# Optimization experiments

Hardware: AMD Instinct MI355X
Metric: run time of the kernel (lower is better)

Reference implementation:

```python
import jax, jax.numpy as jnp
import numpy as np
from jax import lax

B, N, C, T = 32, 1000, 32, 24
K, F_CHEB, F_TIME = 3, 64, 64


def setup_inputs() -> dict:
    key = jax.random.key(0)
    ks = jax.random.split(key, 7)
    return {
        "x": jax.random.normal(ks[0], (B, N, C, T), dtype=jnp.float32),
        "cheb_T": jax.random.normal(ks[1], (K, N, N), dtype=jnp.float32) * (1.0 / np.sqrt(N)),
        "Theta": jax.random.normal(ks[2], (K, C, F_CHEB), dtype=jnp.float32) * 0.1,
        "time_w": jax.random.normal(ks[3], (F_TIME, F_CHEB, 1, 3), dtype=jnp.float32) * 0.05,
        "time_b": jax.random.normal(ks[4], (F_TIME,), dtype=jnp.float32) * 0.05,
        "res_w": jax.random.normal(ks[5], (F_TIME, C, 1, 1), dtype=jnp.float32) * 0.1,
        "res_b": jax.random.normal(ks[6], (F_TIME,), dtype=jnp.float32) * 0.05,
    }


def _conv2d(x, w, stride_t, pad_t):
    # x: [B, Cin, N, T] (NCHW with H=nodes, W=time), w: [Cout, Cin, kh, kw]
    return lax.conv_general_dilated(
        x, w, window_strides=(1, stride_t), padding=((0, 0), (pad_t, pad_t)),
        dimension_numbers=("NCHW", "OIHW", "NCHW"))


def reference(x, cheb_T, Theta, time_w, time_b, res_w, res_b):
    # ChebConv: rhs_k[b,n,c,t] = sum_m T_k[m,n] x[b,m,c,t]; out = sum_k rhs_k @ Theta_k
    # Fused over all timesteps and polynomial orders in one einsum.
    spatial = jax.nn.relu(
        jnp.einsum("knm,bmct,kcf->bnft", cheb_T, x, Theta))  # [B,N,F_cheb,T]
    # time conv over the T axis (kernel (1,3), pad (0,1), stride (1,1))
    h = spatial.transpose(0, 2, 1, 3)  # [B,F_cheb,N,T]
    tc = _conv2d(h, time_w, 1, 1) + time_b[None, :, None, None]
    tc = jnp.tanh(tc) * jax.nn.sigmoid(tc)  # wave-net gating
    # 1x1 residual conv on the raw input (Dropout output in source is unused)
    res = _conv2d(x.transpose(0, 2, 1, 3), res_w, 1, 0) + res_b[None, :, None, None]
    out = (res + tc).transpose(0, 2, 1, 3)  # [B,N,F_time,T]
    return out
```

## Files before the change

kernel.cpp:

```cpp
#include <hip/hip_runtime.h>
#include <math.h>

typedef __attribute__((ext_vector_type(4))) float f32x4;
typedef __attribute__((ext_vector_type(16))) float f32x16;
typedef __attribute__((ext_vector_type(8))) short s16x8;
typedef __attribute__((ext_vector_type(8))) unsigned short u16x8;
typedef __attribute__((ext_vector_type(4))) unsigned short u16x4;

#define NB 32
#define NN 1000
#define NT 24
#define NP 1024
#define TCN 768

#define GLOAD16(g, l) __builtin_amdgcn_global_load_lds( \
    (const __attribute__((address_space(1))) unsigned int*)(g), \
    (__attribute__((address_space(3))) unsigned int*)(l), 16, 0, 0)

__device__ __forceinline__ unsigned short f2bf(float f){
  union { float fv; unsigned int u; } v; v.fv = f;
  unsigned int r = v.u + 0x7FFFu + ((v.u >> 16) & 1u);
  return (unsigned short)(r >> 16);
}

__global__ void k0_cheb(const float* __restrict__ cheb, unsigned short* __restrict__ cbT){
  int idx = blockIdx.x * 256 + threadIdx.x;
  int base = idx << 2;
  int m = base & (NP - 1);
  int r = base >> 10;
  int n = r & (NP - 1);
  int k = r >> 10;
  u16x4 o = (u16x4){0,0,0,0};
  if (n < NN && m < NN){
    if (m + 3 < NN){
      f32x4 v = *(const f32x4*)(cheb + ((size_t)k*NN + n)*NN + m);
      o[0] = f2bf(v[0]); o[1] = f2bf(v[1]); o[2] = f2bf(v[2]); o[3] = f2bf(v[3]);
    } else {
      #pragma unroll
      for (int i = 0; i < 4; ++i)
        if (m + i < NN) o[i] = f2bf(cheb[((size_t)k*NN + n)*NN + m + i]);
    }
  }
  *(u16x4*)(cbT + base) = o;
}

__global__ __launch_bounds__(256) void k0_x(const float* __restrict__ x,
                     unsigned short* __restrict__ xbT, unsigned short* __restrict__ xt2){
  __shared__ unsigned short tile[64*770];
  const int b  = blockIdx.x >> 4;
  const int m0 = (blockIdx.x & 15) << 6;
  const int tid = threadIdx.x;
  for (int i = tid; i < 64*192; i += 256){
    int mi = i / 192, c4 = (i - mi*192) << 2;
    f32x4 v = (f32x4){0.f,0.f,0.f,0.f};
    if (m0 + mi < NN) v = *(const f32x4*)(x + (size_t)(b*NN + m0 + mi)*768 + c4);
    unsigned short* tp = tile + mi*770 + c4;
    tp[0] = f2bf(v[0]); tp[1] = f2bf(v[1]); tp[2] = f2bf(v[2]); tp[3] = f2bf(v[3]);
  }
  __syncthreads();
  {
    const int seg = tid & 7, r0 = tid >> 3;
    for (int rr = 0; rr < 768; rr += 32){
      int r = rr + r0;
      int t = r >> 5, c = r & 31, ct = c*24 + t;
      u16x8 v;
      #pragma unroll
      for (int e = 0; e < 8; ++e) v[e] = tile[(seg*8 + e)*770 + ct];
      *(u16x8*)(xbT + ((size_t)b*TCN + r)*NP + m0 + seg*8) = v;
    }
  }
  if (m0 < NN){
    int rows = NN - m0; if (rows > 64) rows = 64;
    for (int i = tid; i < rows*96; i += 256){
      int mi = i / 96, s = i - mi*96;
      u16x8 v;
      #pragma unroll
      for (int e = 0; e < 8; ++e){
        int r = s*8 + e; int t = r >> 5, c = r & 31;
        v[e] = tile[mi*770 + c*24 + t];
      }
      *(u16x8*)(xt2 + (size_t)(b*NN + m0 + mi)*TCN + s*8) = v;
    }
  }
}

__global__ void k0_w(const float* __restrict__ Theta, const float* __restrict__ tw,
                     const float* __restrict__ rw,
                     unsigned short* __restrict__ ThT, unsigned short* __restrict__ WtT,
                     unsigned short* __restrict__ rwT){
  int i = blockIdx.x * 256 + threadIdx.x;
  if (i < 64*96){
    int f = i / 96, kc = i - f*96;
    ThT[i] = f2bf(Theta[kc*64 + f]);
  }
  if (i < 64*192){
    int f = i / 192, kk = i - f*192;
    int dt = kk >> 6, fi = kk & 63;
    WtT[i] = f2bf(tw[(f*64 + fi)*3 + dt]);
  }
  if (i < 64*32){
    rwT[i] = f2bf(rw[i]);
  }
}

__global__ __launch_bounds__(256, 3) void k1_cheb_theta(
    const unsigned short* __restrict__ cbT,
    const unsigned short* __restrict__ xbT,
    const unsigned short* __restrict__ ThT,
    unsigned short* __restrict__ spa)
{
  __shared__ __align__(16) unsigned short smem[20480];

  int pB = blockIdx.x;
  int lb = (pB & 7) * 384 + (pB >> 3);
  const int tcb = lb % 6; lb /= 6;
  const int nt  = lb & 15;
  const int b   = lb >> 4;

  const int tid  = threadIdx.x;
  const int wid  = tid >> 6;
  const int lane = tid & 63;
  const int l31  = lane & 31;
  const int h    = lane >> 5;
  const int wr   = wid >> 1;
  const int wc   = wid & 1;

  const int rl4 = lane >> 2;
  const int swz = (((lane & 3) ^ ((rl4 >> 1) & 3)) << 3);
  const unsigned short* baseA = cbT + (size_t)(nt*64 + rl4)*NP + swz;
  const unsigned short* baseB = xbT + ((size_t)b*TCN + tcb*128 + rl4)*NP + swz;
  char* smc = (char*)smem;

  const int s_rd = (l31 >> 1) & 3;
  const int ch0 = ((h ^ s_rd) << 3);
  const int ch1 = (((2 + h) ^ s_rd) << 3);

  f32x16 acc[3][2];
  #pragma unroll
  for (int k = 0; k < 3; ++k)
    #pragma unroll
    for (int j = 0; j < 2; ++j)
      #pragma unroll
      for (int r = 0; r < 16; ++r) acc[k][j][r] = 0.f;

  const int rA  = wr*32 + l31;
  const int rB0 = wc*64 + l31;

  {
    #pragma unroll
    for (int q = 0; q < 5; ++q){
      const int g = wid*5 + q;
      if (g < 12){
        const int k = g >> 2, rg = g & 3;
        GLOAD16(baseA + (size_t)k*NP*NP + rg*16*NP, smc + k*4096 + rg*1024);
      } else {
        const int rg = g - 12;
        GLOAD16(baseB + (size_t)rg*16*NP, smc + 12288 + rg*1024);
      }
    }
  }
  __syncthreads();

  int cur = 0;
  for (int step = 0; step < 32; ++step){
    if (step < 31){
      const int so = (step + 1) << 5;
      const int bo = (cur ^ 1) * 20480;
      #pragma unroll
      for (int q = 0; q < 5; ++q){
        const int g = wid*5 + q;
        if (g < 12){
          const int k = g >> 2, rg = g & 3;
          GLOAD16(baseA + (size_t)k*NP*NP + rg*16*NP + so, smc + bo + k*4096 + rg*1024);
        } else {
          const int rg = g - 12;
          GLOAD16(baseB + (size_t)rg*16*NP + so, smc + bo + 12288 + rg*1024);
        }
      }
    }
    const unsigned short* sb = smem + cur*10240;
    #pragma unroll
    for (int ks = 0; ks < 2; ++ks){
      const int ch = ks ? ch1 : ch0;
      s16x8 bf0 = *(const s16x8*)(sb + 6144 + rB0*32 + ch);
      s16x8 bf1 = *(const s16x8*)(sb + 6144 + (rB0 + 32)*32 + ch);
      #pragma unroll
      for (int k = 0; k < 3; ++k){
        s16x8 af = *(const s16x8*)(sb + k*2048 + rA*32 + ch);
        acc[k][0] = __builtin_amdgcn_mfma_f32_32x32x16_bf16(af, bf0, acc[k][0], 0, 0, 0);
        acc[k][1] = __builtin_amdgcn_mfma_f32_32x32x16_bf16(af, bf1, acc[k][1], 0, 0, 0);
      }
    }
    __syncthreads();
    cur ^= 1;
  }

  s16x8 b2[3][2];
  const int fE = wc*32 + l31;
  #pragma unroll
  for (int ch = 0; ch < 3; ++ch)
    #pragma unroll
    for (int ks = 0; ks < 2; ++ks)
      b2[ch][ks] = *(const s16x8*)(ThT + fE*96 + ch*32 + ks*16 + h*8);

  unsigned short* yl = smem;
  const int rowE = wr*32 + l31;
  #pragma unroll
  for (int p = 0; p < 4; ++p){
    __syncthreads();
    if (wc == (p >> 1)){
      const int jj = p & 1;
      #pragma unroll
      for (int k = 0; k < 3; ++k)
        #pragma unroll
        for (int r = 0; r < 16; ++r){
          const int nl = wr*32 + (r & 3) + ((r >> 2) << 3) + (h << 2);
          const int kc = k*32 + l31;
          const int q  = kc >> 3;
          yl[nl*104 + (((q ^ (nl & 3)) << 3) | (kc & 7))] = f2bf(acc[k][jj][r]);
        }
    }
    __syncthreads();
    f32x16 a2c;
    #pragma unroll
    for (int r = 0; r < 16; ++r) a2c[r] = 0.f;
    #pragma unroll
    for (int ch = 0; ch < 3; ++ch)
      #pragma unroll
      for (int ks = 0; ks < 2; ++ks){
        const int q = ch*4 + ks*2 + h;
        s16x8 a2 = *(const s16x8*)(yl + rowE*104 + ((q ^ (rowE & 3)) << 3));
        a2c = __builtin_amdgcn_mfma_f32_32x32x16_bf16(a2, b2[ch][ks], a2c, 0, 0, 0);
      }
    const int t = tcb*4 + p;
    #pragma unroll
    for (int r = 0; r < 16; ++r){
      const int nl = wr*32 + (r & 3) + ((r >> 2) << 3) + (h << 2);
      const int n  = nt*64 + nl;
      if (n < NN)
        spa[((size_t)(b*NN + n)*NT + t)*64 + fE] = f2bf(fmaxf(a2c[r], 0.f));
    }
  }
}

__global__ __launch_bounds__(512, 4) void k2_out(
    const unsigned short* __restrict__ spa, const unsigned short* __restrict__ xt2,
    const unsigned short* __restrict__ WtT, const unsigned short* __restrict__ rwT,
    const float* __restrict__ tb, const float* __restrict__ rb,
    float* __restrict__ out)
{
  __shared__ float ylds[8][64*33];
  const int tid  = threadIdx.x;
  const int wid  = tid >> 6;
  const int lane = tid & 63;
  const int l31  = lane & 31;
  const int h    = lane >> 5;
  float* my = &ylds[wid][0];

  const int wbase = (blockIdx.x * 8 + wid) * 96;
  const float tb0 = tb[l31], tb1 = tb[32 + l31];
  const float rb0 = rb[l31], rb1 = rb[32 + l31];

  #pragma unroll
  for (int g = 0; g < 3; ++g){
    const int rg0  = wbase + g*32;
    const int rowA = rg0 + l31;
    const int tA = rowA % 24;
    const int bn = rowA / 24;

    f32x16 atc[2], ars[2];
    #pragma unroll
    for (int r = 0; r < 16; ++r){ atc[0][r]=0.f; atc[1][r]=0.f; ars[0][r]=0.f; ars[1][r]=0.f; }

    #pragma unroll
    for (int s = 0; s < 12; ++s){
      const int dt = s >> 2;
      const int ts = tA + dt - 1;
      s16x8 a = (s16x8){0,0,0,0,0,0,0,0};
      if (ts >= 0 && ts < 24)
        a = *(const s16x8*)(spa + ((size_t)(bn*24 + ts)) * 64 + (s & 3)*16 + h*8);
      s16x8 b0 = *(const s16x8*)(WtT + (size_t)l31*192 + s*16 + h*8);
      s16x8 b1 = *(const s16x8*)(WtT + (size_t)(32 + l31)*192 + s*16 + h*8);
      atc[0] = __builtin_amdgcn_mfma_f32_32x32x16_bf16(a, b0, atc[0], 0, 0, 0);
      atc[1] = __builtin_amdgcn_mfma_f32_32x32x16_bf16(a, b1, atc[1], 0, 0, 0);
    }
    #pragma unroll
    for (int s = 0; s < 2; ++s){
      s16x8 a = *(const s16x8*)(xt2 + (size_t)bn*768 + tA*32 + s*16 + h*8);
      s16x8 b0 = *(const s16x8*)(rwT + (size_t)l31*32 + s*16 + h*8);
      s16x8 b1 = *(const s16x8*)(rwT + (size_t)(32 + l31)*32 + s*16 + h*8);
      ars[0] = __builtin_amdgcn_mfma_f32_32x32x16_bf16(a, b0, ars[0], 0, 0, 0);
      ars[1] = __builtin_amdgcn_mfma_f32_32x32x16_bf16(a, b1, ars[1], 0, 0, 0);
    }

    #pragma unroll
    for (int jn = 0; jn < 2; ++jn){
      const float tbv = jn ? tb1 : tb0;
      const float rbv = jn ? rb1 : rb0;
      const int f = jn*32 + l31;
      #pragma unroll
      for (int r = 0; r < 16; ++r){
        const int tl = (r & 3) + ((r >> 2) << 3) + (h << 2);
        float z = atc[jn][r] + tbv;
        float e = __expf(-z);
        float p = (1.f - e) * __builtin_amdgcn_rcpf(1.f + e*e);
        my[f*33 + tl] = ars[jn][r] + rbv + p;
      }
    }
    #pragma unroll
    for (int c = 0; c < 8; ++c){
      const int row = rg0 + c*4;
      const int t   = row % 24;
      const int bnw = row / 24;
      f32x4 v = *(const f32x4*)(my + lane*33 + c*4);
      *(f32x4*)(out + ((size_t)bnw*64 + lane)*24 + t) = v;
    }
  }
}

extern "C" void kernel_launch(void* const* d_in, const int* in_sizes, int n_in,
                              void* d_out, int out_size, void* d_ws, size_t ws_size,
                              hipStream_t stream) {
  const float* x     = (const float*)d_in[0];
  const float* cheb  = (const float*)d_in[1];
  const float* Theta = (const float*)d_in[2];
  const float* tw    = (const float*)d_in[3];
  const float* tb    = (const float*)d_in[4];
  const float* rw    = (const float*)d_in[5];
  const float* rb    = (const float*)d_in[6];
  float* out = (float*)d_out;

  char* ws = (char*)d_ws;
  size_t off = 0;
  auto alloc = [&](size_t bytes) -> void* {
    void* p = ws + off;
    off += (bytes + 255) & ~(size_t)255;
    return p;
  };
  unsigned short* cbT = (unsigned short*)alloc((size_t)3*NP*NP*2);
  unsigned short* xbT = (unsigned short*)alloc((size_t)NB*TCN*NP*2);
  unsigned short* xt2 = (unsigned short*)alloc((size_t)NB*NN*TCN*2);
  unsigned short* spa = (unsigned short*)alloc((size_t)NB*NN*NT*64*2);
  unsigned short* ThT = (unsigned short*)alloc((size_t)64*96*2);
  unsigned short* WtT = (unsigned short*)alloc((size_t)64*192*2);
  unsigned short* rwT = (unsigned short*)alloc((size_t)64*32*2);

  hipLaunchKernelGGL(k0_cheb, dim3(3072), dim3(256), 0, stream, cheb, cbT);
  hipLaunchKernelGGL(k0_x,    dim3(512),  dim3(256), 0, stream, x, xbT, xt2);
  hipLaunchKernelGGL(k0_w,    dim3(48),   dim3(256), 0, stream, Theta, tw, rw, ThT, WtT, rwT);
  hipLaunchKernelGGL(k1_cheb_theta, dim3(32*16*6), dim3(256), 0, stream, cbT, xbT, ThT, spa);
  hipLaunchKernelGGL(k2_out,  dim3(1000), dim3(512), 0, stream, spa, xt2, WtT, rwT, tb, rb, out);
}
```

Before: 481.3 us.

## Stage k2 inputs in swizzled LDS via async loads and store outputs directly

The output kernel now copies each block's 16 (b,n) cells of spatial features and transposed input into LDS with global_load_lds, using an XOR swizzle. The temporal-conv and residual MFMAs then read their A operands from LDS, and the t±1 halo is handled by clamping the row and masking lanes. The LDS transpose staging of outputs is removed; each lane writes 4 consecutive timesteps as float4 straight to global. The launch changes to 2000 blocks of 256 threads. Global loads become coalesced but the output writes are more scattered.

```diff
diff --git a/kernel.cpp b/kernel.cpp
--- a/kernel.cpp
+++ b/kernel.cpp
@@ -243,77 +243,95 @@
   }
 }
 
-__global__ __launch_bounds__(512, 4) void k2_out(
+__global__ __launch_bounds__(256, 2) void k2_out(
     const unsigned short* __restrict__ spa, const unsigned short* __restrict__ xt2,
     const unsigned short* __restrict__ WtT, const unsigned short* __restrict__ rwT,
     const float* __restrict__ tb, const float* __restrict__ rb,
     float* __restrict__ out)
 {
-  __shared__ float ylds[8][64*33];
+  __shared__ __align__(16) unsigned short sst[36864];
+  const unsigned short* spa_s = sst;
+  const unsigned short* xt2_s = sst + 24576;
+
+  const int c0   = blockIdx.x * 16;
   const int tid  = threadIdx.x;
-  const int wid  = tid >> 6;
+  const int w    = tid >> 6;
   const int lane = tid & 63;
   const int l31  = lane & 31;
   const int h    = lane >> 5;
-  float* my = &ylds[wid][0];
-
-  const int wbase = (blockIdx.x * 8 + wid) * 96;
-  const float tb0 = tb[l31], tb1 = tb[32 + l31];
-  const float rb0 = rb[l31], rb1 = rb[32 + l31];
+  char* smc = (char*)sst;
+
+  const unsigned short* gs = spa + (size_t)c0 * 1536;
+  const unsigned short* gx = xt2 + (size_t)c0 * 768;
+  #pragma unroll
+  for (int it = 0; it < 12; ++it){
+    const int row = it*32 + (tid >> 3);
+    const int sc  = (tid & 7) ^ (row & 7);
+    GLOAD16(gs + (size_t)row*64 + sc*8, smc + it*4096 + w*1024);
+  }
+  #pragma unroll
+  for (int it = 0; it < 6; ++it){
+    const int row = it*64 + (tid >> 2);
+    const int sc  = (tid & 3) ^ ((row >> 1) & 3);
+    GLOAD16(gx + (size_t)row*32 + sc*8, smc + 49152 + it*4096 + w*1024);
+  }
+  __syncthreads();
+
+  const float tb0v = tb[l31], tb1v = tb[32 + l31];
+  const float rb0v = rb[l31], rb1v = rb[32 + l31];
 
   #pragma unroll
   for (int g = 0; g < 3; ++g){
-    const int rg0  = wbase + g*32;
-    const int rowA = rg0 + l31;
-    const int tA = rowA % 24;
-    const int bn = rowA / 24;
-
-    f32x16 atc[2], ars[2];
-    #pragma unroll
-    for (int r = 0; r < 16; ++r){ atc[0][r]=0.f; atc[1][r]=0.f; ars[0][r]=0.f; ars[1][r]=0.f; }
+    const int rbase = w*96 + g*32;
+    const int r = rbase + l31;
+    const int cell = r / 24;
+    const int t = r - cell*24;
+
+    f32x16 a0, a1, rs0, rs1;
+    #pragma unroll
+    for (int e = 0; e < 16; ++e){ a0[e]=0.f; a1[e]=0.f; rs0[e]=0.f; rs1[e]=0.f; }
 
     #pragma unroll
     for (int s = 0; s < 12; ++s){
       const int dt = s >> 2;
-      const int ts = tA + dt - 1;
-      s16x8 a = (s16x8){0,0,0,0,0,0,0,0};
-      if (ts >= 0 && ts < 24)
-        a = *(const s16x8*)(spa + ((size_t)(bn*24 + ts)) * 64 + (s & 3)*16 + h*8);
+      const int tv = t + dt - 1;
+      int ar = r + dt - 1;
+      ar = ar < 0 ? 0 : (ar > 383 ? 383 : ar);
+      const int cfi = ((s & 3) << 1) + h;
+      s16x8 a = *(const s16x8*)(spa_s + (size_t)ar*64 + ((cfi ^ (ar & 7)) << 3));
+      if (!((unsigned)tv < 24u)) a = (s16x8){0,0,0,0,0,0,0,0};
       s16x8 b0 = *(const s16x8*)(WtT + (size_t)l31*192 + s*16 + h*8);
       s16x8 b1 = *(const s16x8*)(WtT + (size_t)(32 + l31)*192 + s*16 + h*8);
-      atc[0] = __builtin_amdgcn_mfma_f32_32x32x16_bf16(a, b0, atc[0], 0, 0, 0);
-      atc[1] = __builtin_amdgcn_mfma_f32_32x32x16_bf16(a, b1, atc[1], 0, 0, 0);
+      a0 = __builtin_amdgcn_mfma_f32_32x32x16_bf16(a, b0, a0, 0, 0, 0);
+      a1 = __builtin_amdgcn_mfma_f32_32x32x16_bf16(a, b1, a1, 0, 0, 0);
     }
     #pragma unroll
     for (int s = 0; s < 2; ++s){
-      s16x8 a = *(const s16x8*)(xt2 + (size_t)bn*768 + tA*32 + s*16 + h*8);
+      const int cres = (s << 1) + h;
+      s16x8 a = *(const s16x8*)(xt2_s + (size_t)r*32 + ((cres ^ ((r >> 1) & 3)) << 3));
       s16x8 b0 = *(const s16x8*)(rwT + (size_t)l31*32 + s*16 + h*8);
       s16x8 b1 = *(const s16x8*)(rwT + (size_t)(32 + l31)*32 + s*16 + h*8);
-      ars[0] = __builtin_amdgcn_mfma_f32_32x32x16_bf16(a, b0, ars[0], 0, 0, 0);
-      ars[1] = __builtin_amdgcn_mfma_f32_32x32x16_bf16(a, b1, ars[1], 0, 0, 0);
-    }
-
-    #pragma unroll
-    for (int jn = 0; jn < 2; ++jn){
-      const float tbv = jn ? tb1 : tb0;
-      const float rbv = jn ? rb1 : rb0;
-      const int f = jn*32 + l31;
-      #pragma unroll
-      for (int r = 0; r < 16; ++r){
-        const int tl = (r & 3) + ((r >> 2) << 3) + (h << 2);
-        float z = atc[jn][r] + tbv;
-        float e = __expf(-z);
-        float p = (1.f - e) * __builtin_amdgcn_rcpf(1.f + e*e);
-        my[f*33 + tl] = ars[jn][r] + rbv + p;
-      }
-    }
-    #pragma unroll
-    for (int c = 0; c < 8; ++c){
-      const int row = rg0 + c*4;
-      const int t   = row % 24;
-      const int bnw = row / 24;
-      f32x4 v = *(const f32x4*)(my + lane*33 + c*4);
-      *(f32x4*)(out + ((size_t)bnw*64 + lane)*24 + t) = v;
+      rs0 = __builtin_amdgcn_mfma_f32_32x32x16_bf16(a, b0, rs0, 0, 0, 0);
+      rs1 = __builtin_amdgcn_mfma_f32_32x32x16_bf16(a, b1, rs1, 0, 0, 0);
+    }
+
+    #pragma unroll
+    for (int q = 0; q < 4; ++q){
+      const int rq = rbase + q*8 + 4*h;
+      const int cq = rq / 24;
+      const int tq = rq - cq*24;
+      f32x4 v0, v1;
+      #pragma unroll
+      for (int e = 0; e < 4; ++e){
+        float z0 = a0[q*4 + e] + tb0v;
+        float e0 = __expf(-z0);
+        v0[e] = rs0[q*4 + e] + rb0v + (1.f - e0) * __builtin_amdgcn_rcpf(1.f + e0*e0);
+        float z1 = a1[q*4 + e] + tb1v;
+        float e1 = __expf(-z1);
+        v1[e] = rs1[q*4 + e] + rb1v + (1.f - e1) * __builtin_amdgcn_rcpf(1.f + e1*e1);
+      }
+      *(f32x4*)(out + ((size_t)(c0 + cq)*64 + l31)*24 + tq)      = v0;
+      *(f32x4*)(out + ((size_t)(c0 + cq)*64 + 32 + l31)*24 + tq) = v1;
     }
   }
 }
@@ -349,5 +367,5 @@
   hipLaunchKernelGGL(k0_x,    dim3(512),  dim3(256), 0, stream, x, xbT, xt2);
   hipLaunchKernelGGL(k0_w,    dim3(48),   dim3(256), 0, stream, Theta, tw, rw, ThT, WtT, rwT);
   hipLaunchKernelGGL(k1_cheb_theta, dim3(32*16*6), dim3(256), 0, stream, cbT, xbT, ThT, spa);
-  hipLaunchKernelGGL(k2_out,  dim3(1000), dim3(512), 0, stream, spa, xt2, WtT, rwT, tb, rb, out);
-}
+  hipLaunchKernelGGL(k2_out,  dim3(2000), dim3(256), 0, stream, spa, xt2, WtT, rwT, tb, rb, out);
+}
```

After: 391.8 us. 18.6% less time.
